# Performance work log

Hardware: AMD Instinct MI355X
Metric: run time of the kernel (lower is better)

Reference implementation:

```python
import jax, jax.numpy as jnp
import numpy as np

VOCAB, EMB, HID, K = 50000, 256, 512, 20
START, END = 18, 19
B, T = 32, 256
NEG = -10000.0


def _lstm(x, Wih, Whh, bih, bhh):
    # x: [T, B, E] -> outputs [T, B, H]; PyTorch gate order i,f,g,o
    Bn = x.shape[1]
    H = Whh.shape[1]

    def step(carry, xt):
        h, c = carry
        z = xt @ Wih.T + h @ Whh.T + bih + bhh
        i, f, g, o = jnp.split(z, 4, axis=-1)
        c = jax.nn.sigmoid(f) * c + jax.nn.sigmoid(i) * jnp.tanh(g)
        h = jax.nn.sigmoid(o) * jnp.tanh(c)
        return (h, c), h

    init = (jnp.zeros((Bn, H), x.dtype), jnp.zeros((Bn, H), x.dtype))
    _, hs = jax.lax.scan(step, init, x)
    return hs


def setup_inputs() -> dict:
    key = jax.random.key(0)
    ks = jax.random.split(key, 10)
    sentence = jax.random.randint(ks[0], (B, T), 0, VOCAB, dtype=jnp.int32)
    lengths = jax.random.randint(ks[1], (B,), 1, T + 1, dtype=jnp.int32).at[0].set(T)
    s = 0.05
    emb = jax.random.normal(ks[2], (VOCAB, EMB), jnp.float32) * s
    Wf_ih = jax.random.normal(ks[3], (4 * HID, EMB), jnp.float32) * s
    Wf_hh = jax.random.normal(ks[4], (4 * HID, HID), jnp.float32) * s
    Wb_ih = jax.random.normal(ks[5], (4 * HID, EMB), jnp.float32) * s
    Wb_hh = jax.random.normal(ks[6], (4 * HID, HID), jnp.float32) * s
    bf_ih = jnp.zeros((4 * HID,), jnp.float32)
    bf_hh = jnp.zeros((4 * HID,), jnp.float32)
    bb_ih = jnp.zeros((4 * HID,), jnp.float32)
    bb_hh = jnp.zeros((4 * HID,), jnp.float32)
    Wout = jax.random.normal(ks[7], (K, 2 * HID), jnp.float32) * s
    bout = jnp.zeros((K,), jnp.float32)
    transitions = jax.random.normal(ks[8], (K, K), jnp.float32)
    transitions = transitions.at[START, :].set(NEG).at[:, END].set(NEG)
    return dict(sentence=sentence, lengths=lengths, emb=emb,
                Wf_ih=Wf_ih, Wf_hh=Wf_hh, bf_ih=bf_ih, bf_hh=bf_hh,
                Wb_ih=Wb_ih, Wb_hh=Wb_hh, bb_ih=bb_ih, bb_hh=bb_hh,
                Wout=Wout, bout=bout, transitions=transitions)


def reference(sentence, lengths, emb, Wf_ih, Wf_hh, bf_ih, bf_hh,
              Wb_ih, Wb_hh, bb_ih, bb_hh, Wout, bout, transitions):
    Bn, Tn = sentence.shape
    Kt = transitions.shape[0]
    t = jnp.arange(Tn)
    valid = t[None, :] < lengths[:, None]  # [B,T]

    # --- BiLSTM features (packed semantics: dropout in eval mode = identity) ---
    x = emb[sentence]  # [B,T,E]
    hf = _lstm(x.transpose(1, 0, 2), Wf_ih, Wf_hh, bf_ih, bf_hh).transpose(1, 0, 2)
    # backward dir: reverse each sequence within its own length (pack_padded semantics)
    rev_idx = jnp.where(valid, lengths[:, None] - 1 - t[None, :], t[None, :])  # [B,T]
    ridx = jnp.broadcast_to(rev_idx[:, :, None], x.shape)
    xb = jnp.take_along_axis(x, ridx, axis=1)
    hb_rev = _lstm(xb.transpose(1, 0, 2), Wb_ih, Wb_hh, bb_ih, bb_hh).transpose(1, 0, 2)
    hb = jnp.take_along_axis(hb_rev, jnp.broadcast_to(rev_idx[:, :, None], hb_rev.shape), axis=1)
    lstm_out = jnp.concatenate([hf, hb], axis=-1) * valid[:, :, None]  # pad_packed zeros pads
    feats = lstm_out @ Wout.T + bout  # [B,T,K]

    # --- Viterbi ---
    init_fv = jnp.full((Bn, Kt), NEG, feats.dtype).at[:, START].set(0.0)

    def step(fv, feat):
        # scores[b, next, prev] = fv[b, prev] + transitions[next, prev]
        scores = fv[:, None, :] + transitions[None, :, :]
        bptr = jnp.argmax(scores, axis=2)  # [B,K]
        best = jnp.take_along_axis(scores, bptr[:, :, None], axis=2)[:, :, 0]
        fv_new = best + feat
        return fv_new, (fv_new, bptr)

    _, (fvt, bptrs) = jax.lax.scan(step, init_fv, feats.transpose(1, 0, 2))
    fvt = fvt.transpose(1, 0, 2)      # [B,T,K]
    bptrs = bptrs.transpose(1, 0, 2)  # [B,T,K]

    last = (lengths - 1).astype(jnp.int32)[:, None, None]
    final_fv = jnp.take_along_axis(fvt, jnp.broadcast_to(last, (Bn, 1, Kt)), axis=1)[:, 0, :]
    terminal = final_fv + transitions[END]  # [B,K]
    best_tag = jnp.argmax(terminal, axis=1)  # [B]
    path_score = jnp.take_along_axis(terminal, best_tag[:, None], axis=1)  # [B,1]

    # right-align backpointers per sample; prepend sentinel column of value K
    bptrs_ext = jnp.concatenate([bptrs, jnp.full((Bn, Tn, 1), Kt, bptrs.dtype)], axis=-1)  # [B,T,K+1]
    src = t[None, :] - (Tn - lengths)[:, None]  # [B,T]
    g = jnp.take_along_axis(bptrs_ext,
                            jnp.broadcast_to(jnp.clip(src, 0, Tn - 1)[:, :, None], bptrs_ext.shape),
                            axis=1)
    aligned = jnp.where((src >= 0)[:, :, None], g, Kt)  # [B,T,K+1]

    def back_step(bt, bp_t):
        bt_new = jnp.take_along_axis(bp_t, bt[:, None], axis=1)[:, 0]
        return bt_new, bt_new

    _, path_ts = jax.lax.scan(back_step, best_tag.astype(bptrs.dtype),
                              aligned.transpose(1, 0, 2), reverse=True)  # [T,B]
    best_path = jnp.concatenate([path_ts.T, best_tag[:, None].astype(bptrs.dtype)], axis=1)  # [B,T+1]
    return path_score, best_path
```

## Files before the change

### kernel.cpp

```cpp
#include <hip/hip_runtime.h>
#include <math.h>

#define VOCAB 50000
#define EMB 256
#define HID 512
#define KTAGS 20
#define START_TAG 18
#define END_TAG 19
#define BB 32
#define TT 256
#define NEGV -10000.0f
#define HSROW 644
#define XSROW 264

__device__ __forceinline__ float sigmoidf_(float x) { return 1.0f / (1.0f + expf(-x)); }

__global__ __launch_bounds__(512, 4) void k_lstm_persist(
    const int* __restrict__ lengths,
    const int* __restrict__ sentence,
    const float* __restrict__ emb,
    const float* __restrict__ Wf_hh, const float* __restrict__ Wb_hh,
    const float* __restrict__ Wf_ih, const float* __restrict__ Wb_ih,
    const float* __restrict__ bf_ih, const float* __restrict__ bf_hh,
    const float* __restrict__ bb_ih, const float* __restrict__ bb_hh,
    float* __restrict__ hping,
    unsigned* __restrict__ flags,
    float* __restrict__ hbuf)
{
    const int wg = blockIdx.x;
    const int dir = wg >> 8;
    const int slice = (wg & 255) >> 2;
    const int grp = wg & 3;
    const int tid = threadIdx.x;
    const int wave = tid >> 6;
    const int lane = tid & 63;
    const int u_glob = slice * 8 + wave;

    const float* Whh  = dir ? Wb_hh : Wf_hh;
    const float* WihP = dir ? Wb_ih : Wf_ih;
    const float* bihP = dir ? bb_ih : bf_ih;
    const float* bhhP = dir ? bb_hh : bf_hh;

    float4 wD[4][2];
    #pragma unroll
    for (int c = 0; c < 4; c++) {
        const float4* wr = (const float4*)(Whh + (size_t)(c * HID + u_glob) * HID + lane * 8);
        wD[c][0] = wr[0]; wD[c][1] = wr[1];
    }
    float4 iD[4];
    #pragma unroll
    for (int c = 0; c < 4; c++)
        iD[c] = *(const float4*)(WihP + (size_t)(c * HID + u_glob) * EMB + lane * 4);
    float bc[4];
    #pragma unroll
    for (int c = 0; c < 4; c++)
        bc[c] = bihP[c * HID + u_glob] + bhhP[c * HID + u_glob];

    __shared__ float hs[8 * HSROW];
    __shared__ float xs[8 * XSROW];
    __shared__ float zw[8 * 132];
    __shared__ int stok[8][TT];
    __shared__ int lens_raw[32];
    __shared__ int order_s[32];
    __shared__ int lens_s[32];
    __shared__ int nbt_s[TT];

    if (tid < 32) lens_raw[tid] = lengths[tid];
    __syncthreads();
    if (tid < 32) {
        int me = lens_raw[tid], rank = 0;
        #pragma unroll 4
        for (int o = 0; o < 32; o++) {
            int lo = lens_raw[o];
            rank += (lo > me || (lo == me && o < tid)) ? 1 : 0;
        }
        order_s[rank] = tid;
        lens_s[rank] = me;
    }
    if (tid >= 256) {
        int t = tid - 256, c = 0;
        #pragma unroll 4
        for (int b = 0; b < 32; b++) c += (lens_raw[b] > t) ? 1 : 0;
        nbt_s[t] = c;
    }
    __syncthreads();
    for (int i = tid; i < 8 * TT; i += 512) {
        int j = i >> 8, c = i & 255;
        stok[j][c] = sentence[order_s[grp * 8 + j] * TT + c];
    }
    __syncthreads();

    const int tlimit = lens_s[grp * 8];

    const int gj = lane & 7;
    const int g_act = (lane < 8);
    const int p_sort = grp * 8 + gj;
    const int mylen = lens_s[p_sort];
    const int mybat = order_s[p_sort];
    float* hout = hbuf + (size_t)(dir * BB + mybat) * TT * HID + u_glob;
    float* hp   = hping + (size_t)dir * BB * HID + (size_t)mybat * HID + u_glob;

    const int kq = tid & 127;
    const int rA = tid >> 7;
    const int wbBase = 4 * kq + 4 * (kq >> 2);
    const int sb_lo = order_s[grp * 8 + rA];
    const int sb_hi = order_s[grp * 8 + rA + 4];
    const int sb0   = order_s[grp * 8];
    const size_t o_lo = (size_t)sb_lo * 2048 + (size_t)kq * 16;
    const size_t o_hi = (size_t)sb_hi * 2048 + (size_t)kq * 16;
    const size_t o_fb = (size_t)sb0   * 2048 + (size_t)kq * 16;

    const int xrow = tid >> 6;
    const int xpart = tid & 63;
    const int xlen = lens_s[grp * 8 + xrow];
    float* xdst = &xs[xrow * XSROW + xpart * 4];

    const int rdoff = 8 * lane + 4 * (lane >> 1);

    float cS = 0.f;
    unsigned* myflag = flags + ((size_t)(dir * 4 + grp) * 64 + slice) * 16;
    const unsigned* pollbase = flags + (size_t)(dir * 4 + grp) * 64 * 16;

#define DOTRED()                                                               \
    for (int j = 0; j < jmax; j++) {                                           \
        const float* hb = &hs[j * HSROW + rdoff];                              \
        float4 h0 = *(const float4*)(hb);                                      \
        float4 h1 = *(const float4*)(hb + 4);                                  \
        float4 xv = *(const float4*)&xs[j * XSROW + lane * 4];                 \
        float a0 = 0.f, a1 = 0.f, a2 = 0.f, a3 = 0.f;                          \
        a0 = fmaf(wD[0][0].x, h0.x, a0); a0 = fmaf(wD[0][0].y, h0.y, a0);      \
        a0 = fmaf(wD[0][0].z, h0.z, a0); a0 = fmaf(wD[0][0].w, h0.w, a0);      \
        a0 = fmaf(wD[0][1].x, h1.x, a0); a0 = fmaf(wD[0][1].y, h1.y, a0);      \
        a0 = fmaf(wD[0][1].z, h1.z, a0); a0 = fmaf(wD[0][1].w, h1.w, a0);      \
        a0 = fmaf(iD[0].x, xv.x, a0);    a0 = fmaf(iD[0].y, xv.y, a0);         \
        a0 = fmaf(iD[0].z, xv.z, a0);    a0 = fmaf(iD[0].w, xv.w, a0);         \
        a1 = fmaf(wD[1][0].x, h0.x, a1); a1 = fmaf(wD[1][0].y, h0.y, a1);      \
        a1 = fmaf(wD[1][0].z, h0.z, a1); a1 = fmaf(wD[1][0].w, h0.w, a1);      \
        a1 = fmaf(wD[1][1].x, h1.x, a1); a1 = fmaf(wD[1][1].y, h1.y, a1);      \
        a1 = fmaf(wD[1][1].z, h1.z, a1); a1 = fmaf(wD[1][1].w, h1.w, a1);      \
        a1 = fmaf(iD[1].x, xv.x, a1);    a1 = fmaf(iD[1].y, xv.y, a1);         \
        a1 = fmaf(iD[1].z, xv.z, a1);    a1 = fmaf(iD[1].w, xv.w, a1);         \
        a2 = fmaf(wD[2][0].x, h0.x, a2); a2 = fmaf(wD[2][0].y, h0.y, a2);      \
        a2 = fmaf(wD[2][0].z, h0.z, a2); a2 = fmaf(wD[2][0].w, h0.w, a2);      \
        a2 = fmaf(wD[2][1].x, h1.x, a2); a2 = fmaf(wD[2][1].y, h1.y, a2);      \
        a2 = fmaf(wD[2][1].z, h1.z, a2); a2 = fmaf(wD[2][1].w, h1.w, a2);      \
        a2 = fmaf(iD[2].x, xv.x, a2);    a2 = fmaf(iD[2].y, xv.y, a2);         \
        a2 = fmaf(iD[2].z, xv.z, a2);    a2 = fmaf(iD[2].w, xv.w, a2);         \
        a3 = fmaf(wD[3][0].x, h0.x, a3); a3 = fmaf(wD[3][0].y, h0.y, a3);      \
        a3 = fmaf(wD[3][0].z, h0.z, a3); a3 = fmaf(wD[3][0].w, h0.w, a3);      \
        a3 = fmaf(wD[3][1].x, h1.x, a3); a3 = fmaf(wD[3][1].y, h1.y, a3);      \
        a3 = fmaf(wD[3][1].z, h1.z, a3); a3 = fmaf(wD[3][1].w, h1.w, a3);      \
        a3 = fmaf(iD[3].x, xv.x, a3);    a3 = fmaf(iD[3].y, xv.y, a3);         \
        a3 = fmaf(iD[3].z, xv.z, a3);    a3 = fmaf(iD[3].w, xv.w, a3);         \
        bool lo32 = (lane & 32) == 0;                                          \
        float tA = __shfl_xor(lo32 ? a2 : a0, 32);                             \
        float tB = __shfl_xor(lo32 ? a3 : a1, 32);                             \
        float rAq = (lo32 ? a0 : a2) + tA;                                     \
        float rBq = (lo32 ? a1 : a3) + tB;                                     \
        bool lo16 = (lane & 16) == 0;                                          \
        float tC = __shfl_xor(lo16 ? rBq : rAq, 16);                           \
        float r  = (lo16 ? rAq : rBq) + tC;                                    \
        r += __shfl_xor(r, 8);                                                 \
        r += __shfl_xor(r, 4);                                                 \
        r += __shfl_xor(r, 2);                                                 \
        r += __shfl_xor(r, 1);                                                 \
        if ((lane & 15) == 0)                                                  \
            zw[wave * 132 + (lane >> 4) * 33 + j] = r;                         \
    }

    for (int t = 0; t < tlimit; t++) {
        const int nbt = nbt_s[t];
        const int jmax = min(max(nbt - grp * 8, 0), 8);
        const int act = g_act && (t < mylen);
        const int pred_lo = (grp * 8 + rA < nbt);
        const int pred_hi = (grp * 8 + rA + 4 < nbt);

        int posx = dir ? ((t < xlen) ? xlen - 1 - t : t) : t;
        const float* xr = emb + (size_t)stok[xrow][posx] * EMB + xpart * 4;
        float4 xa = *(const float4*)xr;

        if (t > 0 && wave == 0) {
            const unsigned tgt = (unsigned)t;
            const unsigned* cp = pollbase + lane * 16;
            bool mydone = false;
            while (true) {
                if (!mydone)
                    mydone = __hip_atomic_load(cp, __ATOMIC_RELAXED,
                                               __HIP_MEMORY_SCOPE_AGENT) >= tgt;
                if (__ballot(mydone) == ~0ull) break;
                __builtin_amdgcn_s_sleep(1);
            }
        }
        __syncthreads();

        {
            const char* baseD = (const char*)hping
                + ((size_t)(t & 1) * 2 * BB * HID + (size_t)dir * BB * HID) * 4;
            const char* fb = baseD + o_fb;
            const char* a0 = pred_lo ? baseD + o_lo : fb;
            const char* a1 = pred_hi ? baseD + o_hi : fb;
            float4 u0, u1;
            asm volatile(
                "global_load_dwordx4 %0, %2, off sc0 sc1\n\t"
                "global_load_dwordx4 %1, %3, off sc0 sc1\n\t"
                "s_waitcnt vmcnt(0)"
                : "=&v"(u0), "=&v"(u1)
                : "v"(a0), "v"(a1)
                : "memory");
            *(float4*)&hs[(rA    ) * HSROW + wbBase] = u0;
            *(float4*)&hs[(rA + 4) * HSROW + wbBase] = u1;
            *(float4*)xdst = xa;
        }
        __syncthreads();

        DOTRED();

        float hn = 0.f;
        if (act) {
            float iv = zw[wave * 132 +  0 + gj] + bc[0];
            float fv = zw[wave * 132 + 33 + gj] + bc[1];
            float gv = zw[wave * 132 + 66 + gj] + bc[2];
            float ov = zw[wave * 132 + 99 + gj] + bc[3];
            float cn = sigmoidf_(fv) * cS + sigmoidf_(iv) * tanhf(gv);
            hn = sigmoidf_(ov) * tanhf(cn);
            cS = cn;
            __hip_atomic_store(hp + (size_t)(((t + 1) & 1) * 2) * BB * HID, hn,
                               __ATOMIC_RELAXED, __HIP_MEMORY_SCOPE_AGENT);
        }

        __syncthreads();
        if (t < tlimit - 1 && tid == 0)
            __hip_atomic_store(myflag, (unsigned)(t + 1),
                               __ATOMIC_RELAXED, __HIP_MEMORY_SCOPE_AGENT);

        if (act) hout[(size_t)t * HID] = hn;
    }
#undef DOTRED
}

__global__ __launch_bounds__(256) void k_feats(
    const int* __restrict__ lengths,
    const float* __restrict__ hbuf,
    const float* __restrict__ Wout,
    const float* __restrict__ bout,
    float* __restrict__ feats)
{
    const int w = threadIdx.x >> 6;
    const int lane = threadIdx.x & 63;
    const int idx = blockIdx.x * 4 + w;
    const int b = idx >> 8, t = idx & 255;
    const int len = lengths[b];

    __shared__ float red[4][64][21];

    float acc[KTAGS];
    bool active = (t < len);
    if (active) {
        const int ofs = lane * 16;
        const float* src = (ofs < HID)
            ? hbuf + ((size_t)b * TT + t) * HID + ofs
            : hbuf + ((size_t)(BB + b) * TT + (len - 1 - t)) * HID + (ofs - HID);
        float x[16];
        #pragma unroll
        for (int q = 0; q < 4; q++) {
            float4 v = *(const float4*)(src + 4 * q);
            x[4 * q] = v.x; x[4 * q + 1] = v.y; x[4 * q + 2] = v.z; x[4 * q + 3] = v.w;
        }
        #pragma unroll
        for (int k = 0; k < KTAGS; k++) {
            const float* wr = Wout + (size_t)k * (2 * HID) + ofs;
            float a = 0.f;
            #pragma unroll
            for (int q = 0; q < 4; q++) {
                float4 v = *(const float4*)(wr + 4 * q);
                a = fmaf(x[4 * q], v.x, a);
                a = fmaf(x[4 * q + 1], v.y, a);
                a = fmaf(x[4 * q + 2], v.z, a);
                a = fmaf(x[4 * q + 3], v.w, a);
            }
            acc[k] = a;
        }
    } else {
        #pragma unroll
        for (int k = 0; k < KTAGS; k++) acc[k] = 0.f;
    }
    #pragma unroll
    for (int k = 0; k < KTAGS; k++) red[w][lane][k] = acc[k];
    __syncthreads();

    if (active && lane < KTAGS) {
        float s = bout[lane];
        #pragma unroll 8
        for (int l = 0; l < 64; l++) s += red[w][l][lane];
        feats[(size_t)idx * KTAGS + lane] = s;
    }
}

__global__ __launch_bounds__(64) void k_viterbi(
    const int* __restrict__ lengths,
    const float* __restrict__ trans,
    const float* __restrict__ feats,
    float* __restrict__ out)
{
    const int b = blockIdx.x;
    const int len = lengths[b];
    const int tid = threadIdx.x;

    __shared__ float tr[KTAGS * KTAGS];
    __shared__ float fvb[2][KTAGS];
    __shared__ int   bp[TT][KTAGS];
    __shared__ float term[KTAGS];

    for (int i = tid; i < KTAGS * KTAGS; i += 64) tr[i] = trans[i];
    if (tid < KTAGS) fvb[0][tid] = (tid == START_TAG) ? 0.f : NEGV;
    __syncthreads();

    float ft = (tid < KTAGS) ? feats[((size_t)b * TT) * KTAGS + tid] : 0.f;
    for (int t = 0; t < len; t++) {
        float ftn = (tid < KTAGS && t + 1 < len)
                  ? feats[((size_t)b * TT + t + 1) * KTAGS + tid] : 0.f;
        if (tid < KTAGS) {
            const float* fvc = fvb[t & 1];
            float best = -1e30f; int bi = 0;
            #pragma unroll
            for (int p = 0; p < KTAGS; p++) {
                float s = fvc[p] + tr[tid * KTAGS + p];
                if (s > best) { best = s; bi = p; }
            }
            fvb[(t + 1) & 1][tid] = best + ft;
            bp[t][tid] = bi;
        }
        ft = ftn;
        __syncthreads();
    }

    if (tid < KTAGS) term[tid] = fvb[len & 1][tid] + tr[END_TAG * KTAGS + tid];
    __syncthreads();

    if (tid == 0) {
        int bt_ = 0; float best = term[0];
        for (int k = 1; k < KTAGS; k++)
            if (term[k] > best) { best = term[k]; bt_ = k; }
        out[b] = best;
        float* path = out + BB + (size_t)b * (TT + 1);
        path[TT] = (float)bt_;
        int cur = bt_;
        for (int t = TT - 1; t >= 0; t--) {
            int src = t - (TT - len);
            if (src >= 0) cur = bp[src][cur];
            else          cur = KTAGS;
            path[t] = (float)cur;
        }
    }
}

extern "C" void kernel_launch(void* const* d_in, const int* in_sizes, int n_in,
                              void* d_out, int out_size, void* d_ws, size_t ws_size,
                              hipStream_t stream) {
    const int*   sentence = (const int*)d_in[0];
    const int*   lengths  = (const int*)d_in[1];
    const float* emb      = (const float*)d_in[2];
    const float* Wf_ih    = (const float*)d_in[3];
    const float* Wf_hh    = (const float*)d_in[4];
    const float* bf_ih    = (const float*)d_in[5];
    const float* bf_hh    = (const float*)d_in[6];
    const float* Wb_ih    = (const float*)d_in[7];
    const float* Wb_hh    = (const float*)d_in[8];
    const float* bb_ih    = (const float*)d_in[9];
    const float* bb_hh    = (const float*)d_in[10];
    const float* Wout     = (const float*)d_in[11];
    const float* bout     = (const float*)d_in[12];
    const float* trans    = (const float*)d_in[13];
    float* out = (float*)d_out;

    float*    hping = (float*)d_ws;
    unsigned* flags = (unsigned*)((char*)d_ws + 262144);
    float*    hbuf  = (float*)((char*)d_ws + 262144 + 32768);
    float*    feats = hbuf + (size_t)2 * BB * TT * HID;

    (void)hipMemsetAsync(d_ws, 0, 262144 + 32768, stream);

    hipLaunchKernelGGL(k_lstm_persist, dim3(512), dim3(512), 0, stream,
                       lengths, sentence, emb, Wf_hh, Wb_hh, Wf_ih, Wb_ih,
                       bf_ih, bf_hh, bb_ih, bb_hh, hping, flags, hbuf);
    hipLaunchKernelGGL(k_feats, dim3(BB * TT / 4), dim3(256), 0, stream,
                       lengths, hbuf, Wout, bout, feats);
    hipLaunchKernelGGL(k_viterbi, dim3(BB), dim3(64), 0, stream,
                       lengths, trans, feats, out);
}
```

Measured before the change: 1.793 ms.

## Hoist input projection before the flag wait and replace the end-of-step barrier with an LDS counter

Each step now loads the next timestep's embedding row early and computes the W_ih·x partial sums for all 8 rows before polling the cross-block flags. This takes the input projection off the serial recurrent critical path, leaving only the W_hh·h dot products after the wait. The trailing __syncthreads before publishing the step flag is replaced by an LDS atomic counter, so the last wave to finish stores the flag while the other waves continue. The cost is more registers for the eight float4 partials, which can hurt occupancy, plus subtler ordering of the flag publication.

After: 3.266 ms. +82.2%, slower.

```diff
diff --git a/kernel.cpp b/kernel.cpp
--- a/kernel.cpp
+++ b/kernel.cpp
@@ -64,8 +64,10 @@
     __shared__ int order_s[32];
     __shared__ int lens_s[32];
     __shared__ int nbt_s[TT];
+    __shared__ unsigned lds_cnt;
 
     if (tid < 32) lens_raw[tid] = lengths[tid];
+    if (tid == 33) lds_cnt = 0u;
     __syncthreads();
     if (tid < 32) {
         int me = lens_raw[tid], rank = 0;
@@ -121,52 +123,12 @@
     unsigned* myflag = flags + ((size_t)(dir * 4 + grp) * 64 + slice) * 16;
     const unsigned* pollbase = flags + (size_t)(dir * 4 + grp) * 64 * 16;
 
-#define DOTRED()                                                               \
-    for (int j = 0; j < jmax; j++) {                                           \
-        const float* hb = &hs[j * HSROW + rdoff];                              \
-        float4 h0 = *(const float4*)(hb);                                      \
-        float4 h1 = *(const float4*)(hb + 4);                                  \
-        float4 xv = *(const float4*)&xs[j * XSROW + lane * 4];                 \
-        float a0 = 0.f, a1 = 0.f, a2 = 0.f, a3 = 0.f;                          \
-        a0 = fmaf(wD[0][0].x, h0.x, a0); a0 = fmaf(wD[0][0].y, h0.y, a0);      \
-        a0 = fmaf(wD[0][0].z, h0.z, a0); a0 = fmaf(wD[0][0].w, h0.w, a0);      \
-        a0 = fmaf(wD[0][1].x, h1.x, a0); a0 = fmaf(wD[0][1].y, h1.y, a0);      \
-        a0 = fmaf(wD[0][1].z, h1.z, a0); a0 = fmaf(wD[0][1].w, h1.w, a0);      \
-        a0 = fmaf(iD[0].x, xv.x, a0);    a0 = fmaf(iD[0].y, xv.y, a0);         \
-        a0 = fmaf(iD[0].z, xv.z, a0);    a0 = fmaf(iD[0].w, xv.w, a0);         \
-        a1 = fmaf(wD[1][0].x, h0.x, a1); a1 = fmaf(wD[1][0].y, h0.y, a1);      \
-        a1 = fmaf(wD[1][0].z, h0.z, a1); a1 = fmaf(wD[1][0].w, h0.w, a1);      \
-        a1 = fmaf(wD[1][1].x, h1.x, a1); a1 = fmaf(wD[1][1].y, h1.y, a1);      \
-        a1 = fmaf(wD[1][1].z, h1.z, a1); a1 = fmaf(wD[1][1].w, h1.w, a1);      \
-        a1 = fmaf(iD[1].x, xv.x, a1);    a1 = fmaf(iD[1].y, xv.y, a1);         \
-        a1 = fmaf(iD[1].z, xv.z, a1);    a1 = fmaf(iD[1].w, xv.w, a1);         \
-        a2 = fmaf(wD[2][0].x, h0.x, a2); a2 = fmaf(wD[2][0].y, h0.y, a2);      \
-        a2 = fmaf(wD[2][0].z, h0.z, a2); a2 = fmaf(wD[2][0].w, h0.w, a2);      \
-        a2 = fmaf(wD[2][1].x, h1.x, a2); a2 = fmaf(wD[2][1].y, h1.y, a2);      \
-        a2 = fmaf(wD[2][1].z, h1.z, a2); a2 = fmaf(wD[2][1].w, h1.w, a2);      \
-        a2 = fmaf(iD[2].x, xv.x, a2);    a2 = fmaf(iD[2].y, xv.y, a2);         \
-        a2 = fmaf(iD[2].z, xv.z, a2);    a2 = fmaf(iD[2].w, xv.w, a2);         \
-        a3 = fmaf(wD[3][0].x, h0.x, a3); a3 = fmaf(wD[3][0].y, h0.y, a3);      \
-        a3 = fmaf(wD[3][0].z, h0.z, a3); a3 = fmaf(wD[3][0].w, h0.w, a3);      \
-        a3 = fmaf(wD[3][1].x, h1.x, a3); a3 = fmaf(wD[3][1].y, h1.y, a3);      \
-        a3 = fmaf(wD[3][1].z, h1.z, a3); a3 = fmaf(wD[3][1].w, h1.w, a3);      \
-        a3 = fmaf(iD[3].x, xv.x, a3);    a3 = fmaf(iD[3].y, xv.y, a3);         \
-        a3 = fmaf(iD[3].z, xv.z, a3);    a3 = fmaf(iD[3].w, xv.w, a3);         \
-        bool lo32 = (lane & 32) == 0;                                          \
-        float tA = __shfl_xor(lo32 ? a2 : a0, 32);                             \
-        float tB = __shfl_xor(lo32 ? a3 : a1, 32);                             \
-        float rAq = (lo32 ? a0 : a2) + tA;                                     \
-        float rBq = (lo32 ? a1 : a3) + tB;                                     \
-        bool lo16 = (lane & 16) == 0;                                          \
-        float tC = __shfl_xor(lo16 ? rBq : rAq, 16);                           \
-        float r  = (lo16 ? rAq : rBq) + tC;                                    \
-        r += __shfl_xor(r, 8);                                                 \
-        r += __shfl_xor(r, 4);                                                 \
-        r += __shfl_xor(r, 2);                                                 \
-        r += __shfl_xor(r, 1);                                                 \
-        if ((lane & 15) == 0)                                                  \
-            zw[wave * 132 + (lane >> 4) * 33 + j] = r;                         \
-    }
+    {
+        int posx = dir ? (xlen - 1) : 0;
+        const float* xr = emb + (size_t)stok[xrow][posx] * EMB + xpart * 4;
+        *(float4*)xdst = *(const float4*)xr;
+    }
+    __syncthreads();
 
     for (int t = 0; t < tlimit; t++) {
         const int nbt = nbt_s[t];
@@ -175,9 +137,29 @@
         const int pred_lo = (grp * 8 + rA < nbt);
         const int pred_hi = (grp * 8 + rA + 4 < nbt);
 
-        int posx = dir ? ((t < xlen) ? xlen - 1 - t : t) : t;
-        const float* xr = emb + (size_t)stok[xrow][posx] * EMB + xpart * 4;
-        float4 xa = *(const float4*)xr;
+        float4 xa;
+        {
+            int tp = (t + 1 < tlimit) ? t + 1 : t;
+            int posn = dir ? ((tp < xlen) ? xlen - 1 - tp : tp) : tp;
+            const float* xrn = emb + (size_t)stok[xrow][posn] * EMB + xpart * 4;
+            xa = *(const float4*)xrn;
+        }
+
+        float4 zxp[8];
+        #pragma unroll
+        for (int j = 0; j < 8; j++) {
+            float4 xv = *(const float4*)&xs[j * XSROW + lane * 4];
+            float4 p;
+            p.x = iD[0].x * xv.x; p.x = fmaf(iD[0].y, xv.y, p.x);
+            p.x = fmaf(iD[0].z, xv.z, p.x); p.x = fmaf(iD[0].w, xv.w, p.x);
+            p.y = iD[1].x * xv.x; p.y = fmaf(iD[1].y, xv.y, p.y);
+            p.y = fmaf(iD[1].z, xv.z, p.y); p.y = fmaf(iD[1].w, xv.w, p.y);
+            p.z = iD[2].x * xv.x; p.z = fmaf(iD[2].y, xv.y, p.z);
+            p.z = fmaf(iD[2].z, xv.z, p.z); p.z = fmaf(iD[2].w, xv.w, p.z);
+            p.w = iD[3].x * xv.x; p.w = fmaf(iD[3].y, xv.y, p.w);
+            p.w = fmaf(iD[3].z, xv.z, p.w); p.w = fmaf(iD[3].w, xv.w, p.w);
+            zxp[j] = p;
+        }
 
         if (t > 0 && wave == 0) {
             const unsigned tgt = (unsigned)t;
@@ -213,7 +195,42 @@
         }
         __syncthreads();
 
-        DOTRED();
+        for (int j = 0; j < jmax; j++) {
+            const float* hb = &hs[j * HSROW + rdoff];
+            float4 h0 = *(const float4*)(hb);
+            float4 h1 = *(const float4*)(hb + 4);
+            float a0 = zxp[j].x, a1 = zxp[j].y, a2 = zxp[j].z, a3 = zxp[j].w;
+            a0 = fmaf(wD[0][0].x, h0.x, a0); a0 = fmaf(wD[0][0].y, h0.y, a0);
+            a0 = fmaf(wD[0][0].z, h0.z, a0); a0 = fmaf(wD[0][0].w, h0.w, a0);
+            a0 = fmaf(wD[0][1].x, h1.x, a0); a0 = fmaf(wD[0][1].y, h1.y, a0);
+            a0 = fmaf(wD[0][1].z, h1.z, a0); a0 = fmaf(wD[0][1].w, h1.w, a0);
+            a1 = fmaf(wD[1][0].x, h0.x, a1); a1 = fmaf(wD[1][0].y, h0.y, a1);
+            a1 = fmaf(wD[1][0].z, h0.z, a1); a1 = fmaf(wD[1][0].w, h0.w, a1);
+            a1 = fmaf(wD[1][1].x, h1.x, a1); a1 = fmaf(wD[1][1].y, h1.y, a1);
+            a1 = fmaf(wD[1][1].z, h1.z, a1); a1 = fmaf(wD[1][1].w, h1.w, a1);
+            a2 = fmaf(wD[2][0].x, h0.x, a2); a2 = fmaf(wD[2][0].y, h0.y, a2);
+            a2 = fmaf(wD[2][0].z, h0.z, a2); a2 = fmaf(wD[2][0].w, h0.w, a2);
+            a2 = fmaf(wD[2][1].x, h1.x, a2); a2 = fmaf(wD[2][1].y, h1.y, a2);
+            a2 = fmaf(wD[2][1].z, h1.z, a2); a2 = fmaf(wD[2][1].w, h1.w, a2);
+            a3 = fmaf(wD[3][0].x, h0.x, a3); a3 = fmaf(wD[3][0].y, h0.y, a3);
+            a3 = fmaf(wD[3][0].z, h0.z, a3); a3 = fmaf(wD[3][0].w, h0.w, a3);
+            a3 = fmaf(wD[3][1].x, h1.x, a3); a3 = fmaf(wD[3][1].y, h1.y, a3);
+            a3 = fmaf(wD[3][1].z, h1.z, a3); a3 = fmaf(wD[3][1].w, h1.w, a3);
+            bool lo32 = (lane & 32) == 0;
+            float tA = __shfl_xor(lo32 ? a2 : a0, 32);
+            float tB = __shfl_xor(lo32 ? a3 : a1, 32);
+            float rAq = (lo32 ? a0 : a2) + tA;
+            float rBq = (lo32 ? a1 : a3) + tB;
+            bool lo16 = (lane & 16) == 0;
+            float tC = __shfl_xor(lo16 ? rBq : rAq, 16);
+            float r  = (lo16 ? rAq : rBq) + tC;
+            r += __shfl_xor(r, 8);
+            r += __shfl_xor(r, 4);
+            r += __shfl_xor(r, 2);
+            r += __shfl_xor(r, 1);
+            if ((lane & 15) == 0)
+                zw[wave * 132 + (lane >> 4) * 33 + j] = r;
+        }
 
         float hn = 0.f;
         if (act) {
@@ -228,14 +245,16 @@
                                __ATOMIC_RELAXED, __HIP_MEMORY_SCOPE_AGENT);
         }
 
-        __syncthreads();
-        if (t < tlimit - 1 && tid == 0)
-            __hip_atomic_store(myflag, (unsigned)(t + 1),
-                               __ATOMIC_RELAXED, __HIP_MEMORY_SCOPE_AGENT);
+        asm volatile("s_waitcnt vmcnt(0)" ::: "memory");
+        if (lane == 0) {
+            unsigned old = atomicAdd(&lds_cnt, 1u);
+            if (old == (unsigned)(t * 8 + 7) && t < tlimit - 1)
+                __hip_atomic_store(myflag, (unsigned)(t + 1),
+                                   __ATOMIC_RELAXED, __HIP_MEMORY_SCOPE_AGENT);
+        }
 
         if (act) hout[(size_t)t * HID] = hn;
     }
-#undef DOTRED
 }
 
 __global__ __launch_bounds__(256) void k_feats(
```
